# Kernel optimization log

Measured on AMD Instinct MI355X. Metric: run time of the kernel, lower is better.

The kernel has to match this reference:

```python
import jax, jax.numpy as jnp
import numpy as np

T, B, D, H = 1024, 64, 1024, 30  # seq_len, batch, input_size, hidden_size


def setup_inputs() -> dict:
    key = jax.random.key(0)
    ks = jax.random.split(key, 11)
    sc = 1.0 / np.sqrt(H)  # torch default init scale ~ U(-1/sqrt(H), 1/sqrt(H))
    u = lambda k, shape: jax.random.uniform(k, shape, dtype=jnp.float32, minval=-sc, maxval=sc)
    return {
        "x": jax.random.normal(ks[0], (T, B, D), dtype=jnp.float32),
        "W_ih0": u(ks[1], (4 * H, D)),
        "W_hh0": u(ks[2], (4 * H, H)),
        "b_ih0": u(ks[3], (4 * H,)),
        "b_hh0": u(ks[4], (4 * H,)),
        "W_ih1": u(ks[5], (4 * H, H)),
        "W_hh1": u(ks[6], (4 * H, H)),
        "b_ih1": u(ks[7], (4 * H,)),
        "b_hh1": u(ks[8], (4 * H,)),
        "W_out": u(ks[9], (1, H)),
        "b_out": u(ks[10], (1,)),
    }


def _lstm_layer(xs, Wih, Whh, bih, bhh):
    # xs: [T, B, Din] -> hs: [T, B, H]. PyTorch gate order: i, f, g, o.
    xg = jnp.einsum("tbd,gd->tbg", xs, Wih) + (bih + bhh)  # precompute input projection
    h0 = jnp.zeros((xs.shape[1], H), xs.dtype)
    c0 = jnp.zeros((xs.shape[1], H), xs.dtype)

    def step(carry, xw):
        h, c = carry
        gates = xw + h @ Whh.T  # [B, 4H]
        i, f, g, o = jnp.split(gates, 4, axis=-1)
        c = jax.nn.sigmoid(f) * c + jax.nn.sigmoid(i) * jnp.tanh(g)
        h = jax.nn.sigmoid(o) * jnp.tanh(c)
        return (h, c), h

    _, hs = jax.lax.scan(step, (h0, c0), xg)
    return hs


def reference(x, W_ih0, W_hh0, b_ih0, b_hh0, W_ih1, W_hh1, b_ih1, b_hh1, W_out, b_out):
    h1 = _lstm_layer(x, W_ih0, W_hh0, b_ih0, b_hh0)   # layer 0
    h2 = _lstm_layer(h1, W_ih1, W_hh1, b_ih1, b_hh1)  # layer 1
    return h2 @ W_out.T + b_out  # [T, B, 1]
```

## Files before the change

kernel.cpp:

```cpp
#include <hip/hip_runtime.h>
#include <hip/hip_bf16.h>
#include <cstdint>

#define TT 1024
#define BB 64
#define DD 1024
#define HH 30
#define G4 120

#define NPROD 64
#define NROUND 8
#define NCONS 16
#define GBLK 16
#define NGRP 32

typedef __attribute__((ext_vector_type(8))) short short8;
typedef __attribute__((ext_vector_type(4))) float float4v;

__device__ __forceinline__ float frcp(float x) { return __builtin_amdgcn_rcpf(x); }
__device__ __forceinline__ float fsig(float x) { return frcp(1.0f + __expf(-x)); }
__device__ __forceinline__ float ftan(float x) {
    return 2.0f * frcp(1.0f + __expf(-2.0f * x)) - 1.0f;
}
__device__ __forceinline__ float bcast(float v, int l) {
    return __int_as_float(__builtin_amdgcn_readlane(__float_as_int(v), l));
}
__device__ __forceinline__ unsigned short bf16_rne(float f) {
    unsigned u = __float_as_uint(f);
    return (unsigned short)((u + 0x7FFFu + ((u >> 16) & 1u)) >> 16);
}

__global__ void prep_kernel(const float* __restrict__ Wih0,
                            const float* __restrict__ bih0,
                            const float* __restrict__ bhh0,
                            unsigned short* __restrict__ Bhi,
                            unsigned short* __restrict__ Blo,
                            float* __restrict__ bias0,
                            unsigned* __restrict__ cnt) {
    int idx = blockIdx.x * 256 + threadIdx.x;
    int l  = idx & 63;
    int kc = (idx >> 6) & 31;
    int nt = idx >> 11;
    int n = nt * 16 + (l & 15);
    int kb = kc * 32 + (l >> 4) * 8;
    size_t o = (size_t)idx * 8;
#pragma unroll
    for (int j = 0; j < 8; ++j) {
        float wv = (n < G4) ? Wih0[(size_t)n * DD + kb + j] : 0.0f;
        unsigned short hi = bf16_rne(wv);
        float fhi = __uint_as_float((unsigned)hi << 16);
        unsigned short lo = bf16_rne(wv - fhi);
        Bhi[o + j] = hi;
        Blo[o + j] = lo;
    }
    if (idx < 128) bias0[idx] = (idx < G4) ? (bih0[idx] + bhh0[idx]) : 0.0f;
    if (idx < NGRP) cnt[idx] = 0u;
}

template<int Q, bool DO_L1, bool DO_L0>
__device__ __forceinline__ void lstm_step(
    const int t, const int half, const int l, const int b,
    const float (&wa0)[HH], const float (&wb0)[HH],
    const float (&wc1)[HH], const float (&wd1)[HH],
    const float (&we1)[HH], const float (&wf1)[HH],
    const float b1lo, const float b1hi,
    float (&h1b)[HH], float (&h2b)[HH],
    float& c1, float& c2, float2 (&xq)[4],
    const float2* __restrict__ xgptr,
    unsigned& next_g, const unsigned* __restrict__ cnt,
    float* __restrict__ h2buf) {

    float zA = 0.f, zB = 0.f, yA = 0.f, yB = 0.f;
    if (DO_L1) {
        zA = b1lo; yA = b1hi;
#pragma unroll
        for (int j = 0; j < HH; j += 2) {
            zA = fmaf(wc1[j], h1b[j], zA);
            yA = fmaf(wd1[j], h1b[j], yA);
            zB = fmaf(wc1[j + 1], h1b[j + 1], zB);
            yB = fmaf(wd1[j + 1], h1b[j + 1], yB);
        }
#pragma unroll
        for (int j = 0; j < HH; j += 2) {
            zA = fmaf(we1[j], h2b[j], zA);
            yA = fmaf(wf1[j], h2b[j], yA);
            zB = fmaf(we1[j + 1], h2b[j + 1], zB);
            yB = fmaf(wf1[j + 1], h2b[j + 1], yB);
        }
    }

    float h1new = 0.f;
    if (DO_L0) {
        float2 xw = xq[Q];
        const int tn = (t + 4 < TT) ? t + 4 : TT - 1;
        const unsigned gneed = (unsigned)(tn >> 5);
        if (gneed >= next_g) {
            while (__hip_atomic_load(&cnt[gneed], __ATOMIC_ACQUIRE,
                                     __HIP_MEMORY_SCOPE_AGENT) < GBLK)
                __builtin_amdgcn_s_sleep(8);
            next_g = gneed + 1;
        }
        xq[Q] = xgptr[(size_t)tn * (BB * 64)];

        float aA = xw.x, aB = 0.f, cA = xw.y, cB = 0.f;
#pragma unroll
        for (int j = 0; j < HH; j += 2) {
            aA = fmaf(wa0[j], h1b[j], aA);
            cA = fmaf(wb0[j], h1b[j], cA);
            aB = fmaf(wa0[j + 1], h1b[j + 1], aB);
            cB = fmaf(wb0[j + 1], h1b[j + 1], cB);
        }
        float alo = aA + aB, ahi = cA + cB;
        float plo = __shfl_xor(alo, 32, 64);
        float phi = __shfl_xor(ahi, 32, 64);
        float ipre = half ? plo : alo;
        float fpre = half ? alo : plo;
        float gpre = half ? phi : ahi;
        float opre = half ? ahi : phi;
        c1 = fsig(fpre) * c1 + fsig(ipre) * ftan(gpre);
        h1new = fsig(opre) * ftan(c1);
    }

    if (DO_L1) {
        float zlo = zA + zB, zhi = yA + yB;
        float qlo = __shfl_xor(zlo, 32, 64);
        float qhi = __shfl_xor(zhi, 32, 64);
        float ipre = half ? qlo : zlo;
        float fpre = half ? zlo : qlo;
        float gpre = half ? qhi : zhi;
        float opre = half ? zhi : qhi;
        c2 = fsig(fpre) * c2 + fsig(ipre) * ftan(gpre);
        float h2new = fsig(opre) * ftan(c2);
        if (l < HH) h2buf[((size_t)(t - 1) * BB + b) * 32 + l] = h2new;
#pragma unroll
        for (int j = 0; j < HH; ++j) h2b[j] = bcast(h2new, j);
    }
    if (DO_L0) {
#pragma unroll
        for (int j = 0; j < HH; ++j) h1b[j] = bcast(h1new, j);
    }
}

__global__ __launch_bounds__(256) void fused_fwd(
    const float* __restrict__ x, const unsigned short* __restrict__ Bhi,
    const unsigned short* __restrict__ Blo, const float* __restrict__ bias0,
    float* __restrict__ xgp, const float* __restrict__ Whh0,
    const float* __restrict__ Wih1, const float* __restrict__ Whh1,
    const float* __restrict__ bih1, const float* __restrict__ bhh1,
    float* __restrict__ h2buf, unsigned* __restrict__ cnt) {

    const int tid = threadIdx.x;

    if (blockIdx.x < NPROD) {
        const int pb = blockIdx.x;
        const int w = tid >> 6;
        const int l = tid & 63;
        const int lm = l & 15, lq = l >> 4;

        for (int r = 0; r < NROUND; ++r) {
            const int tile = r * NPROD + pb;
            const int r0 = tile * 128 + w * 32;

            float4v acc[2][8];
#pragma unroll
            for (int mt = 0; mt < 2; ++mt)
#pragma unroll
                for (int nt = 0; nt < 8; ++nt) acc[mt][nt] = (float4v)0.0f;

            const float* aptr[2];
            aptr[0] = x + (size_t)(r0 + lm) * DD + lq * 8;
            aptr[1] = x + (size_t)(r0 + 16 + lm) * DD + lq * 8;

            float4 pa[2][2];
#pragma unroll
            for (int mt = 0; mt < 2; ++mt) {
                pa[mt][0] = *(const float4*)(aptr[mt]);
                pa[mt][1] = *(const float4*)(aptr[mt] + 4);
            }

            for (int kc = 0; kc < 32; ++kc) {
                short8 ahi[2], alo[2];
#pragma unroll
                for (int mt = 0; mt < 2; ++mt) {
                    float f[8] = {pa[mt][0].x, pa[mt][0].y, pa[mt][0].z, pa[mt][0].w,
                                  pa[mt][1].x, pa[mt][1].y, pa[mt][1].z, pa[mt][1].w};
#pragma unroll
                    for (int i = 0; i < 8; ++i) {
                        unsigned ub = __float_as_uint(f[i]);
                        ahi[mt][i] = (short)(ub >> 16);
                        float fr = f[i] - __uint_as_float(ub & 0xFFFF0000u);
                        alo[mt][i] = (short)(__float_as_uint(fr) >> 16);
                    }
                }
                if (kc + 1 < 32) {
                    const int ko = (kc + 1) * 32;
#pragma unroll
                    for (int mt = 0; mt < 2; ++mt) {
                        pa[mt][0] = *(const float4*)(aptr[mt] + ko);
                        pa[mt][1] = *(const float4*)(aptr[mt] + ko + 4);
                    }
                }
#pragma unroll
                for (int nt = 0; nt < 8; ++nt) {
                    const size_t bo = ((size_t)(nt * 32 + kc) * 64 + l) * 8;
                    short8 bh = *(const short8*)(Bhi + bo);
                    short8 bl = *(const short8*)(Blo + bo);
                    acc[0][nt] = __builtin_amdgcn_mfma_f32_16x16x32_bf16(ahi[0], bh, acc[0][nt], 0, 0, 0);
                    acc[1][nt] = __builtin_amdgcn_mfma_f32_16x16x32_bf16(ahi[1], bh, acc[1][nt], 0, 0, 0);
                    acc[0][nt] = __builtin_amdgcn_mfma_f32_16x16x32_bf16(alo[0], bh, acc[0][nt], 0, 0, 0);
                    acc[1][nt] = __builtin_amdgcn_mfma_f32_16x16x32_bf16(alo[1], bh, acc[1][nt], 0, 0, 0);
                    acc[0][nt] = __builtin_amdgcn_mfma_f32_16x16x32_bf16(ahi[0], bl, acc[0][nt], 0, 0, 0);
                    acc[1][nt] = __builtin_amdgcn_mfma_f32_16x16x32_bf16(ahi[1], bl, acc[1][nt], 0, 0, 0);
                }
            }

#pragma unroll
            for (int nt = 0; nt < 8; ++nt) {
                const int g = nt * 16 + lm;
                if (g < G4) {
                    const int gm = g % 60;
                    const int lane_t = (gm < HH) ? gm : (32 + gm - HH);
                    const int slot = g / 60;
                    const float bb = bias0[g];
#pragma unroll
                    for (int mt = 0; mt < 2; ++mt)
#pragma unroll
                        for (int i = 0; i < 4; ++i) {
                            const size_t row = r0 + mt * 16 + lq * 4 + i;
                            xgp[(row * 64 + lane_t) * 2 + slot] = acc[mt][nt][i] + bb;
                        }
                }
            }
            __syncthreads();
            if (tid == 0) {
                __threadfence();
                __hip_atomic_fetch_add(&cnt[tile >> 4], 1u, __ATOMIC_RELEASE,
                                       __HIP_MEMORY_SCOPE_AGENT);
            }
        }
        return;
    }

    const int wv = tid >> 6;
    const int l = tid & 63;
    const int b = (blockIdx.x - NPROD) * 4 + wv;
    const int u = l & 31;
    const int half = l >> 5;
    const bool al = (u < HH);
    const int rlo = half * HH + (al ? u : 0);
    const int rhi = 60 + rlo;

    float wa0[HH], wb0[HH], wc1[HH], wd1[HH], we1[HH], wf1[HH];
#pragma unroll
    for (int j = 0; j < HH; ++j) {
        wa0[j] = al ? Whh0[rlo * HH + j] : 0.f;
        wb0[j] = al ? Whh0[rhi * HH + j] : 0.f;
        wc1[j] = al ? Wih1[rlo * HH + j] : 0.f;
        wd1[j] = al ? Wih1[rhi * HH + j] : 0.f;
        we1[j] = al ? Whh1[rlo * HH + j] : 0.f;
        wf1[j] = al ? Whh1[rhi * HH + j] : 0.f;
    }
    const float b1lo = al ? (bih1[rlo] + bhh1[rlo]) : 0.f;
    const float b1hi = al ? (bih1[rhi] + bhh1[rhi]) : 0.f;

    float c1 = 0.f, c2 = 0.f;
    float h1b[HH], h2b[HH];
#pragma unroll
    for (int j = 0; j < HH; ++j) { h1b[j] = 0.f; h2b[j] = 0.f; }

    const float2* xgptr = (const float2*)xgp + (size_t)b * 64 + l;
    float2 xq[4];
    while (__hip_atomic_load(&cnt[0], __ATOMIC_ACQUIRE, __HIP_MEMORY_SCOPE_AGENT) < GBLK)
        __builtin_amdgcn_s_sleep(8);
    unsigned next_g = 1;
#pragma unroll
    for (int p = 0; p < 4; ++p) xq[p] = xgptr[(size_t)p * (BB * 64)];

#define ARGS half, l, b, wa0, wb0, wc1, wd1, we1, wf1, b1lo, b1hi, \
             h1b, h2b, c1, c2, xq, xgptr, next_g, cnt, h2buf

    lstm_step<0, false, true>(0, ARGS);
    for (int t4 = 1; t4 <= TT - 7; t4 += 4) {
        lstm_step<1, true, true>(t4 + 0, ARGS);
        lstm_step<2, true, true>(t4 + 1, ARGS);
        lstm_step<3, true, true>(t4 + 2, ARGS);
        lstm_step<0, true, true>(t4 + 3, ARGS);
    }
    lstm_step<1, true, true>(TT - 3, ARGS);
    lstm_step<2, true, true>(TT - 2, ARGS);
    lstm_step<3, true, true>(TT - 1, ARGS);
    lstm_step<0, true, false>(TT, ARGS);
#undef ARGS
}

__global__ __launch_bounds__(256) void out_proj(
    const float* __restrict__ h2buf, const float* __restrict__ Wout,
    const float* __restrict__ bout, float* __restrict__ out) {
    __shared__ float wos[32];
    if (threadIdx.x < 32)
        wos[threadIdx.x] = (threadIdx.x < HH) ? Wout[threadIdx.x] : 0.0f;
    __syncthreads();
    const int idx = blockIdx.x * 256 + threadIdx.x;
    const float4* hp = (const float4*)(h2buf + (size_t)idx * 32);
    float s0 = 0.f, s1 = 0.f;
#pragma unroll
    for (int q = 0; q < 8; ++q) {
        float4 h = hp[q];
        s0 = fmaf(h.x, wos[q * 4 + 0], s0);
        s1 = fmaf(h.y, wos[q * 4 + 1], s1);
        s0 = fmaf(h.z, wos[q * 4 + 2], s0);
        s1 = fmaf(h.w, wos[q * 4 + 3], s1);
    }
    out[idx] = s0 + s1 + bout[0];
}

extern "C" void kernel_launch(void* const* d_in, const int* in_sizes, int n_in,
                              void* d_out, int out_size, void* d_ws, size_t ws_size,
                              hipStream_t stream) {
    const float* x    = (const float*)d_in[0];
    const float* Wih0 = (const float*)d_in[1];
    const float* Whh0 = (const float*)d_in[2];
    const float* bih0 = (const float*)d_in[3];
    const float* bhh0 = (const float*)d_in[4];
    const float* Wih1 = (const float*)d_in[5];
    const float* Whh1 = (const float*)d_in[6];
    const float* bih1 = (const float*)d_in[7];
    const float* bhh1 = (const float*)d_in[8];
    const float* Wout = (const float*)d_in[9];
    const float* bout = (const float*)d_in[10];
    float* out = (float*)d_out;

    char* ws = (char*)d_ws;
    unsigned short* Bhi = (unsigned short*)ws;
    unsigned short* Blo = (unsigned short*)(ws + 262144);
    float* bias0 = (float*)(ws + 524288);
    unsigned* cnt = (unsigned*)(ws + 524800);
    float* xgp   = (float*)(ws + 1024 * 1024);
    float* h2buf = (float*)(ws + 36 * 1024 * 1024);

    prep_kernel<<<64, 256, 0, stream>>>(Wih0, bih0, bhh0, Bhi, Blo, bias0, cnt);
    fused_fwd<<<NPROD + NCONS, 256, 0, stream>>>(x, Bhi, Blo, bias0, xgp,
                                                 Whh0, Wih1, Whh1, bih1, bhh1,
                                                 h2buf, cnt);
    out_proj<<<256, 256, 0, stream>>>(h2buf, Wout, bout, out);
}
```

Before: 1.078 ms.

## Fuse output projection into recurrent consumers and widen blocks to 512 threads

Folds the final linear projection into the layer-1 step with a wave shuffle reduction, which removes the h2 intermediate buffer and the separate out_proj launch. Blocks grow to 512 threads: consumers handle 8 batches each in 8 blocks, and producers run per-wave tiles that signal completion per wave without a block barrier (counter threshold raised to 64 waves). This cuts launch overhead and global traffic, but adds shuffle work to the serial critical path and changes how consumer waves share CUs.

```diff
diff --git a/kernel.cpp b/kernel.cpp
--- a/kernel.cpp
+++ b/kernel.cpp
@@ -9,9 +9,10 @@
 #define G4 120
 
 #define NPROD 64
-#define NROUND 8
-#define NCONS 16
+#define NROUND 4
+#define NCONS 8
 #define GBLK 16
+#define GDONE 64
 #define NGRP 32
 
 typedef __attribute__((ext_vector_type(8))) short short8;
@@ -64,11 +65,12 @@
     const float (&wc1)[HH], const float (&wd1)[HH],
     const float (&we1)[HH], const float (&wf1)[HH],
     const float b1lo, const float b1hi,
+    const float wosl, const float boutv,
     float (&h1b)[HH], float (&h2b)[HH],
     float& c1, float& c2, float2 (&xq)[4],
     const float2* __restrict__ xgptr,
     unsigned& next_g, const unsigned* __restrict__ cnt,
-    float* __restrict__ h2buf) {
+    float* __restrict__ outp) {
 
     float zA = 0.f, zB = 0.f, yA = 0.f, yB = 0.f;
     if (DO_L1) {
@@ -96,7 +98,7 @@
         const unsigned gneed = (unsigned)(tn >> 5);
         if (gneed >= next_g) {
             while (__hip_atomic_load(&cnt[gneed], __ATOMIC_ACQUIRE,
-                                     __HIP_MEMORY_SCOPE_AGENT) < GBLK)
+                                     __HIP_MEMORY_SCOPE_AGENT) < GDONE)
                 __builtin_amdgcn_s_sleep(8);
             next_g = gneed + 1;
         }
@@ -131,7 +133,13 @@
         float opre = half ? zhi : qhi;
         c2 = fsig(fpre) * c2 + fsig(ipre) * ftan(gpre);
         float h2new = fsig(opre) * ftan(c2);
-        if (l < HH) h2buf[((size_t)(t - 1) * BB + b) * 32 + l] = h2new;
+        float po = wosl * h2new;
+        po += __shfl_xor(po, 1, 64);
+        po += __shfl_xor(po, 2, 64);
+        po += __shfl_xor(po, 4, 64);
+        po += __shfl_xor(po, 8, 64);
+        po += __shfl_xor(po, 16, 64);
+        if (l == 0) outp[(size_t)(t - 1) * BB + b] = po + boutv;
 #pragma unroll
         for (int j = 0; j < HH; ++j) h2b[j] = bcast(h2new, j);
     }
@@ -141,25 +149,28 @@
     }
 }
 
-__global__ __launch_bounds__(256) void fused_fwd(
+__global__ __launch_bounds__(512, 2) void fused_fwd(
     const float* __restrict__ x, const unsigned short* __restrict__ Bhi,
     const unsigned short* __restrict__ Blo, const float* __restrict__ bias0,
     float* __restrict__ xgp, const float* __restrict__ Whh0,
     const float* __restrict__ Wih1, const float* __restrict__ Whh1,
     const float* __restrict__ bih1, const float* __restrict__ bhh1,
-    float* __restrict__ h2buf, unsigned* __restrict__ cnt) {
+    const float* __restrict__ Wout, const float* __restrict__ bout,
+    float* __restrict__ outp, unsigned* __restrict__ cnt) {
 
     const int tid = threadIdx.x;
 
     if (blockIdx.x < NPROD) {
         const int pb = blockIdx.x;
         const int w = tid >> 6;
+        const int wg = w >> 2;
+        const int wl = w & 3;
         const int l = tid & 63;
         const int lm = l & 15, lq = l >> 4;
 
         for (int r = 0; r < NROUND; ++r) {
-            const int tile = r * NPROD + pb;
-            const int r0 = tile * 128 + w * 32;
+            const int tile = r * (NPROD * 2) + pb * 2 + wg;
+            const int r0 = tile * 128 + wl * 32;
 
             float4v acc[2][8];
 #pragma unroll
@@ -231,19 +242,17 @@
                         }
                 }
             }
-            __syncthreads();
-            if (tid == 0) {
-                __threadfence();
+            __threadfence();
+            if (l == 0)
                 __hip_atomic_fetch_add(&cnt[tile >> 4], 1u, __ATOMIC_RELEASE,
                                        __HIP_MEMORY_SCOPE_AGENT);
-            }
         }
         return;
     }
 
     const int wv = tid >> 6;
     const int l = tid & 63;
-    const int b = (blockIdx.x - NPROD) * 4 + wv;
+    const int b = (blockIdx.x - NPROD) * 8 + wv;
     const int u = l & 31;
     const int half = l >> 5;
     const bool al = (u < HH);
@@ -262,6 +271,8 @@
     }
     const float b1lo = al ? (bih1[rlo] + bhh1[rlo]) : 0.f;
     const float b1hi = al ? (bih1[rhi] + bhh1[rhi]) : 0.f;
+    const float wosl = (al && half == 0) ? Wout[u] : 0.f;
+    const float boutv = bout[0];
 
     float c1 = 0.f, c2 = 0.f;
     float h1b[HH], h2b[HH];
@@ -270,14 +281,14 @@
 
     const float2* xgptr = (const float2*)xgp + (size_t)b * 64 + l;
     float2 xq[4];
-    while (__hip_atomic_load(&cnt[0], __ATOMIC_ACQUIRE, __HIP_MEMORY_SCOPE_AGENT) < GBLK)
+    while (__hip_atomic_load(&cnt[0], __ATOMIC_ACQUIRE, __HIP_MEMORY_SCOPE_AGENT) < GDONE)
         __builtin_amdgcn_s_sleep(8);
     unsigned next_g = 1;
 #pragma unroll
     for (int p = 0; p < 4; ++p) xq[p] = xgptr[(size_t)p * (BB * 64)];
 
-#define ARGS half, l, b, wa0, wb0, wc1, wd1, we1, wf1, b1lo, b1hi, \
-             h1b, h2b, c1, c2, xq, xgptr, next_g, cnt, h2buf
+#define ARGS half, l, b, wa0, wb0, wc1, wd1, we1, wf1, b1lo, b1hi, wosl, boutv, \
+             h1b, h2b, c1, c2, xq, xgptr, next_g, cnt, outp
 
     lstm_step<0, false, true>(0, ARGS);
     for (int t4 = 1; t4 <= TT - 7; t4 += 4) {
@@ -291,27 +302,6 @@
     lstm_step<3, true, true>(TT - 1, ARGS);
     lstm_step<0, true, false>(TT, ARGS);
 #undef ARGS
-}
-
-__global__ __launch_bounds__(256) void out_proj(
-    const float* __restrict__ h2buf, const float* __restrict__ Wout,
-    const float* __restrict__ bout, float* __restrict__ out) {
-    __shared__ float wos[32];
-    if (threadIdx.x < 32)
-        wos[threadIdx.x] = (threadIdx.x < HH) ? Wout[threadIdx.x] : 0.0f;
-    __syncthreads();
-    const int idx = blockIdx.x * 256 + threadIdx.x;
-    const float4* hp = (const float4*)(h2buf + (size_t)idx * 32);
-    float s0 = 0.f, s1 = 0.f;
-#pragma unroll
-    for (int q = 0; q < 8; ++q) {
-        float4 h = hp[q];
-        s0 = fmaf(h.x, wos[q * 4 + 0], s0);
-        s1 = fmaf(h.y, wos[q * 4 + 1], s1);
-        s0 = fmaf(h.z, wos[q * 4 + 2], s0);
-        s1 = fmaf(h.w, wos[q * 4 + 3], s1);
-    }
-    out[idx] = s0 + s1 + bout[0];
 }
 
 extern "C" void kernel_launch(void* const* d_in, const int* in_sizes, int n_in,
@@ -336,11 +326,9 @@
     float* bias0 = (float*)(ws + 524288);
     unsigned* cnt = (unsigned*)(ws + 524800);
     float* xgp   = (float*)(ws + 1024 * 1024);
-    float* h2buf = (float*)(ws + 36 * 1024 * 1024);
 
     prep_kernel<<<64, 256, 0, stream>>>(Wih0, bih0, bhh0, Bhi, Blo, bias0, cnt);
-    fused_fwd<<<NPROD + NCONS, 256, 0, stream>>>(x, Bhi, Blo, bias0, xgp,
+    fused_fwd<<<NPROD + NCONS, 512, 0, stream>>>(x, Bhi, Blo, bias0, xgp,
                                                  Whh0, Wih1, Whh1, bih1, bhh1,
-                                                 h2buf, cnt);
-    out_proj<<<256, 256, 0, stream>>>(h2buf, Wout, bout, out);
-}
+                                                 Wout, bout, out, cnt);
+}
```

New measurement: 1.781 ms. +65.2%, slower.
